# Kernel optimization log

Measured on AMD Instinct MI355X. Metric: run time of the kernel, lower is better.

## Reference

```python
import jax, jax.numpy as jnp
import numpy as np
from jax import lax

B, S, E = 1, 8192, 64
KSZ = 2
THRESHOLD = 0.0
GAMMA = 1.0
OUT_DIM = 4


def setup_inputs() -> dict:
    key = jax.random.key(0)
    ks = jax.random.split(key, 12)
    def lin(k, fan_in, fan_out):
        bound = 1.0 / np.sqrt(fan_in)
        kw, kb = jax.random.split(k)
        W = jax.random.uniform(kw, (fan_in, fan_out), jnp.float32, -bound, bound)
        b = jax.random.uniform(kb, (fan_out,), jnp.float32, -bound, bound)
        return W, b
    x = jax.random.normal(ks[0], (B, S, E), jnp.float32)
    cb = 1.0 / np.sqrt(KSZ * KSZ)
    conv_w = jax.random.uniform(ks[1], (1, 1, KSZ, KSZ), jnp.float32, -cb, cb)
    conv_b = jax.random.uniform(ks[2], (1,), jnp.float32, -cb, cb)
    Wq, bq = lin(ks[3], E, E)
    Wk, bk = lin(ks[4], E, E)
    Wv, bv = lin(ks[5], E, E)
    Wp, bp = lin(ks[6], E, OUT_DIM)
    return {"x": x, "conv_w": conv_w, "conv_b": conv_b, "Wq": Wq, "bq": bq,
            "Wk": Wk, "bk": bk, "Wv": Wv, "bv": bv, "Wp": Wp, "bp": bp}


def reference(x, conv_w, conv_b, Wq, bq, Wk, bk, Wv, bv, Wp, bp):
    # conv pre-filter: (B,S,E) -> (B,1,E,S) -> scalar per batch
    patched = jnp.transpose(x, (0, 2, 1))[:, None]  # (B,1,E,S)
    logits = lax.conv_general_dilated(
        patched, conv_w, (1, 1), "VALID",
        dimension_numbers=("NCHW", "OIHW", "NCHW")) + conv_b[None, :, None, None]
    conv_feat = jax.nn.sigmoid(logits - THRESHOLD).mean(axis=(2, 3))  # (B,1)
    conv_feat = conv_feat.reshape(B)[:, None]  # (B,1)

    # classical scaled dot-product attention (note: no output projection in source)
    scale = E ** (-0.5)
    q = x @ Wq + bq
    k = x @ Wk + bk
    v = x @ Wv + bv
    scores = jnp.einsum("bse,bte->bst", q, k) * scale  # (B,S,S)
    attn = jax.nn.softmax(scores, axis=-1)
    attn_out = jnp.einsum("bst,bte->bse", attn, v)  # (B,S,E)

    # RBF reweighting (identically 1 since x==y, computed faithfully)
    diff = attn_out - attn_out
    kernel_vals = jnp.exp(-GAMMA * jnp.sum(diff * diff, axis=-1, keepdims=True))  # (B,S,1)

    weighted = attn_out * conv_feat * kernel_vals  # broadcast valid since B==1
    pooled = weighted.mean(axis=1)  # (B,E)
    return pooled @ Wp + bp  # (B,4)
```

## Files before the change

kernel.cpp:

```cpp
#include <hip/hip_runtime.h>
#include <hip/hip_bf16.h>

#define S_LEN 8192
#define E_DIM 64
#define NCONV (63 * 8191)
#define KSPLIT 32
#define KRANGE (S_LEN / KSPLIT)
#define SVT (S_LEN + 32)
#define KTS 72

typedef short short8 __attribute__((ext_vector_type(8)));
typedef float f32x4 __attribute__((ext_vector_type(4)));

__device__ __forceinline__ float ldin(const void* __restrict__ p, int i, int f32flag) {
    return f32flag ? ((const float*)p)[i]
                   : __bfloat162float(((const __hip_bfloat16*)p)[i]);
}
__device__ __forceinline__ float bfbits2f(unsigned int u16bits) {
    union { unsigned int u; float f; } c; c.u = u16bits << 16; return c.f;
}
__device__ __forceinline__ unsigned short f2bfu(float f) {
    __hip_bfloat16 h = __float2bfloat16(f);
    union { __hip_bfloat16 h; unsigned short u; } c; c.h = h; return c.u;
}
__device__ __forceinline__ int hw_bad(unsigned short h) {
    const unsigned int e = (h >> 7) & 0xFF;
    return !(h == 0 || h == 0x8000 || (e >= 0x60 && e <= 0x86));
}

__global__ __launch_bounds__(256) void qkv_conv(
    const void* __restrict__ x,
    const void* __restrict__ conv_w, const void* __restrict__ conv_b,
    const void* __restrict__ Wq, const void* __restrict__ bq,
    const void* __restrict__ Wk, const void* __restrict__ bk,
    const void* __restrict__ Wv, const void* __restrict__ bv,
    unsigned short* __restrict__ q_bf, unsigned short* __restrict__ k_bf,
    unsigned short* __restrict__ vT_bf, float* __restrict__ conv_part,
    float* __restrict__ l_g, float* __restrict__ w_g,
    float* __restrict__ g_pooled, int* __restrict__ counter)
{
    __shared__ int s_fx, s_fw;
    const int tid = threadIdx.x;
    if (tid == 0) { s_fx = 0; s_fw = 0; }
    __syncthreads();
    if (tid < 64) { if (hw_bad(((const unsigned short*)x)[tid])) atomicOr(&s_fx, 1); }
    else if (tid < 128) { if (hw_bad(((const unsigned short*)Wq)[tid - 64])) atomicOr(&s_fw, 1); }
    __syncthreads();
    const int fx = s_fx, fw = s_fw;

    if (blockIdx.x >= 256) {
        const int bid = blockIdx.x - 256;
        const int gid = bid * 256 + tid;
        if (gid < 8192) { l_g[gid] = 0.f; w_g[gid] = 0.f; }
        if (gid < 64) g_pooled[gid] = 0.f;
        if (gid == 0) *counter = 0;
        const float c0 = ldin(conv_w, 0, fw), c1 = ldin(conv_w, 1, fw);
        const float c2 = ldin(conv_w, 2, fw), c3 = ldin(conv_w, 3, fw);
        const float cb = ldin(conv_b, 0, fw);
        float acc = 0.f;
        for (int idx = gid; idx < NCONV; idx += 64 * 256) {
            const int h = idx % 63;
            const int w = idx / 63;
            const float z = c0 * ldin(x, w * 64 + h, fx)     + c1 * ldin(x, (w + 1) * 64 + h, fx)
                          + c2 * ldin(x, w * 64 + h + 1, fx) + c3 * ldin(x, (w + 1) * 64 + h + 1, fx)
                          + cb;
            acc += 1.f / (1.f + __expf(-z));
        }
        for (int off = 32; off > 0; off >>= 1) acc += __shfl_down(acc, off);
        __shared__ float wsum[4];
        if ((tid & 63) == 0) wsum[tid >> 6] = acc;
        __syncthreads();
        if (tid == 0) conv_part[bid] = wsum[0] + wsum[1] + wsum[2] + wsum[3];
        return;
    }

    __shared__ float wsh[3][4096];
    __shared__ float xT[64 * 16];
    __shared__ float bsh[3][64];
    __shared__ float vs[64 * 17];
    const void* Ws[3] = { Wq, Wk, Wv };
    const void* Bs[3] = { bq, bk, bv };
#pragma unroll
    for (int w = 0; w < 3; ++w) {
        if (fw) {
            const float4* src = (const float4*)Ws[w];
            for (int i = tid; i < 1024; i += 256) {
                float4 v = src[i];
                float* d = &wsh[w][i * 4];
                d[0] = v.x; d[1] = v.y; d[2] = v.z; d[3] = v.w;
            }
            if (tid < 64) bsh[w][tid] = ((const float*)Bs[w])[tid];
        } else {
            const uint4* src = (const uint4*)Ws[w];
            for (int i = tid; i < 512; i += 256) {
                uint4 v = src[i];
                float* d = &wsh[w][i * 8];
                d[0] = bfbits2f(v.x & 0xffff); d[1] = bfbits2f(v.x >> 16);
                d[2] = bfbits2f(v.y & 0xffff); d[3] = bfbits2f(v.y >> 16);
                d[4] = bfbits2f(v.z & 0xffff); d[5] = bfbits2f(v.z >> 16);
                d[6] = bfbits2f(v.w & 0xffff); d[7] = bfbits2f(v.w >> 16);
            }
            if (tid < 64) bsh[w][tid] = bfbits2f(((const unsigned short*)Bs[w])[tid]);
        }
    }

#pragma unroll
    for (int ch = 0; ch < 2; ++ch) {
        const int row0 = blockIdx.x * 32 + ch * 16;
        __syncthreads();
        for (int idx = tid; idx < 1024; idx += 256) {
            const int r = idx >> 6, i = idx & 63;
            xT[i * 16 + r] = ldin(x, (row0 + r) * 64 + i, fx);
        }
        __syncthreads();

        const int e = tid & 63, rg = tid >> 6;
        float aq[4], ak[4], av[4];
#pragma unroll
        for (int r = 0; r < 4; ++r) { aq[r] = bsh[0][e]; ak[r] = bsh[1][e]; av[r] = bsh[2][e]; }
#pragma unroll 8
        for (int i = 0; i < 64; ++i) {
            const float4 xv = *(const float4*)&xT[i * 16 + rg * 4];
            const float wq = wsh[0][i * 64 + e], wk = wsh[1][i * 64 + e], wv = wsh[2][i * 64 + e];
            aq[0] += xv.x * wq; aq[1] += xv.y * wq; aq[2] += xv.z * wq; aq[3] += xv.w * wq;
            ak[0] += xv.x * wk; ak[1] += xv.y * wk; ak[2] += xv.z * wk; ak[3] += xv.w * wk;
            av[0] += xv.x * wv; av[1] += xv.y * wv; av[2] += xv.z * wv; av[3] += xv.w * wv;
        }
#pragma unroll
        for (int r = 0; r < 4; ++r) {
            const int row = row0 + rg * 4 + r;
            q_bf[row * 64 + e] = f2bfu(aq[r] * 0.125f);
            k_bf[row * 64 + e] = f2bfu(ak[r]);
            vs[e * 17 + rg * 4 + r] = av[r];
        }
        __syncthreads();
        {
            const int e2 = tid >> 2, rp = (tid & 3) * 4;
            const unsigned short h0 = f2bfu(vs[e2 * 17 + rp + 0]);
            const unsigned short h1 = f2bfu(vs[e2 * 17 + rp + 1]);
            const unsigned short h2 = f2bfu(vs[e2 * 17 + rp + 2]);
            const unsigned short h3 = f2bfu(vs[e2 * 17 + rp + 3]);
            uint2 pk;
            pk.x = (unsigned int)h0 | ((unsigned int)h1 << 16);
            pk.y = (unsigned int)h2 | ((unsigned int)h3 << 16);
            *(uint2*)(vT_bf + (size_t)e2 * SVT + row0 + rp) = pk;
        }
    }
}

__global__ __launch_bounds__(256) void attn_l(
    const unsigned short* __restrict__ q_bf, const unsigned short* __restrict__ k_bf,
    float* __restrict__ l_g)
{
    __shared__ unsigned short kt[2][32 * KTS];
    const int tid = threadIdx.x;
    const int wave = tid >> 6, lane = tid & 63;
    const int ln = lane & 15, quad = lane >> 4;
    const int qrow0 = blockIdx.x * 256 + wave * 64;
    const int kbase = blockIdx.y * KRANGE;

    short8 aQ[4][2];
#pragma unroll
    for (int T = 0; T < 4; ++T) {
        aQ[T][0] = *(const short8*)(q_bf + (qrow0 + 16 * T + ln) * 64 + quad * 8);
        aQ[T][1] = *(const short8*)(q_bf + (qrow0 + 16 * T + ln) * 64 + 32 + quad * 8);
    }
    const f32x4 zero = {0.f, 0.f, 0.f, 0.f};
    float l_acc[4][4];
#pragma unroll
    for (int T = 0; T < 4; ++T)
#pragma unroll
        for (int r = 0; r < 4; ++r) l_acc[T][r] = 0.f;

    const int krow = tid >> 3, kch = tid & 7;
    uint4 kreg;
    {
        const uint4 k0 = *(const uint4*)(k_bf + (size_t)(kbase + krow) * 64 + kch * 8);
        *(uint4*)(&kt[0][krow * KTS + kch * 8]) = k0;
        kreg = *(const uint4*)(k_bf + (size_t)(kbase + 32 + krow) * 64 + kch * 8);
    }
    __syncthreads();

    const int nIter = KRANGE >> 5;
#pragma unroll 2
    for (int kc = 0; kc < nIter; ++kc) {
        const int cur = kc & 1;
        if (kc + 1 < nIter) *(uint4*)(&kt[cur ^ 1][krow * KTS + kch * 8]) = kreg;
        if (kc + 2 < nIter)
            kreg = *(const uint4*)(k_bf + (size_t)(kbase + (kc + 2) * 32 + krow) * 64 + kch * 8);
        const unsigned short* ktc = &kt[cur][0];
        const short8 bE0 = *(const short8*)(ktc + (2 * ln) * KTS + quad * 8);
        const short8 bE1 = *(const short8*)(ktc + (2 * ln) * KTS + 32 + quad * 8);
        const short8 bO0 = *(const short8*)(ktc + (2 * ln + 1) * KTS + quad * 8);
        const short8 bO1 = *(const short8*)(ktc + (2 * ln + 1) * KTS + 32 + quad * 8);
        f32x4 scE[4], scO[4];
#pragma unroll
        for (int T = 0; T < 4; ++T) {
            scE[T] = __builtin_amdgcn_mfma_f32_16x16x32_bf16(aQ[T][0], bE0, zero, 0, 0, 0);
            scE[T] = __builtin_amdgcn_mfma_f32_16x16x32_bf16(aQ[T][1], bE1, scE[T], 0, 0, 0);
            scO[T] = __builtin_amdgcn_mfma_f32_16x16x32_bf16(aQ[T][0], bO0, zero, 0, 0, 0);
            scO[T] = __builtin_amdgcn_mfma_f32_16x16x32_bf16(aQ[T][1], bO1, scO[T], 0, 0, 0);
        }
#pragma unroll
        for (int T = 0; T < 4; ++T)
#pragma unroll
            for (int r = 0; r < 4; ++r)
                l_acc[T][r] += __expf(scE[T][r]) + __expf(scO[T][r]);
        __syncthreads();
    }

#pragma unroll
    for (int T = 0; T < 4; ++T)
#pragma unroll
        for (int r = 0; r < 4; ++r) {
            float v = l_acc[T][r];
            v += __shfl_xor(v, 1); v += __shfl_xor(v, 2);
            v += __shfl_xor(v, 4); v += __shfl_xor(v, 8);
            if (ln == 0) atomicAdd(&l_g[qrow0 + 16 * T + quad * 4 + r], v);
        }
}

__global__ __launch_bounds__(256) void attn_w(
    const unsigned short* __restrict__ q_bf, const unsigned short* __restrict__ k_bf,
    const float* __restrict__ l_g, float* __restrict__ w_g)
{
    __shared__ unsigned short kt[2][32 * KTS];
    __shared__ float w_sh[4][KRANGE];
    const int tid = threadIdx.x;
    const int wave = tid >> 6, lane = tid & 63;
    const int ln = lane & 15, quad = lane >> 4;
    const int qrow0 = blockIdx.x * 256 + wave * 64;
    const int kbase = blockIdx.y * KRANGE;

    short8 aQ[4][2];
    float lv[4][4];
#pragma unroll
    for (int T = 0; T < 4; ++T) {
        aQ[T][0] = *(const short8*)(q_bf + (qrow0 + 16 * T + ln) * 64 + quad * 8);
        aQ[T][1] = *(const short8*)(q_bf + (qrow0 + 16 * T + ln) * 64 + 32 + quad * 8);
#pragma unroll
        for (int r = 0; r < 4; ++r)
            lv[T][r] = 1.f / l_g[qrow0 + 16 * T + quad * 4 + r];
    }
    const f32x4 zero = {0.f, 0.f, 0.f, 0.f};

    const int krow = tid >> 3, kch = tid & 7;
    uint4 kreg;
    {
        const uint4 k0 = *(const uint4*)(k_bf + (size_t)(kbase + krow) * 64 + kch * 8);
        *(uint4*)(&kt[0][krow * KTS + kch * 8]) = k0;
        kreg = *(const uint4*)(k_bf + (size_t)(kbase + 32 + krow) * 64 + kch * 8);
    }
    __syncthreads();

    const int nIter = KRANGE >> 5;
#pragma unroll 2
    for (int kc = 0; kc < nIter; ++kc) {
        const int cur = kc & 1;
        if (kc + 1 < nIter) *(uint4*)(&kt[cur ^ 1][krow * KTS + kch * 8]) = kreg;
        if (kc + 2 < nIter)
            kreg = *(const uint4*)(k_bf + (size_t)(kbase + (kc + 2) * 32 + krow) * 64 + kch * 8);
        const unsigned short* ktc = &kt[cur][0];
        const short8 bE0 = *(const short8*)(ktc + (2 * ln) * KTS + quad * 8);
        const short8 bE1 = *(const short8*)(ktc + (2 * ln) * KTS + 32 + quad * 8);
        const short8 bO0 = *(const short8*)(ktc + (2 * ln + 1) * KTS + quad * 8);
        const short8 bO1 = *(const short8*)(ktc + (2 * ln + 1) * KTS + 32 + quad * 8);
        f32x4 scE[4], scO[4];
#pragma unroll
        for (int T = 0; T < 4; ++T) {
            scE[T] = __builtin_amdgcn_mfma_f32_16x16x32_bf16(aQ[T][0], bE0, zero, 0, 0, 0);
            scE[T] = __builtin_amdgcn_mfma_f32_16x16x32_bf16(aQ[T][1], bE1, scE[T], 0, 0, 0);
            scO[T] = __builtin_amdgcn_mfma_f32_16x16x32_bf16(aQ[T][0], bO0, zero, 0, 0, 0);
            scO[T] = __builtin_amdgcn_mfma_f32_16x16x32_bf16(aQ[T][1], bO1, scO[T], 0, 0, 0);
        }
        float wE = 0.f, wO = 0.f;
#pragma unroll
        for (int T = 0; T < 4; ++T)
#pragma unroll
            for (int r = 0; r < 4; ++r) {
                wE += __expf(scE[T][r]) * lv[T][r];
                wO += __expf(scO[T][r]) * lv[T][r];
            }
        wE += __shfl_xor(wE, 16); wE += __shfl_xor(wE, 32);
        wO += __shfl_xor(wO, 16); wO += __shfl_xor(wO, 32);
        if (lane < 16) {
            w_sh[wave][kc * 32 + 2 * ln]     = wE;
            w_sh[wave][kc * 32 + 2 * ln + 1] = wO;
        }
        __syncthreads();
    }

    for (int k = tid; k < KRANGE; k += 256)
        atomicAdd(&w_g[kbase + k], w_sh[0][k] + w_sh[1][k] + w_sh[2][k] + w_sh[3][k]);
}

__global__ __launch_bounds__(256) void gemv_final(
    const float* __restrict__ w_g, const unsigned short* __restrict__ vT_bf,
    float* __restrict__ g_pooled, int* __restrict__ counter,
    const float* __restrict__ conv_part,
    const void* __restrict__ Wp, const void* __restrict__ bp,
    const void* __restrict__ x, const void* __restrict__ Wq,
    void* __restrict__ out)
{
    __shared__ float psum[64][5];
    const int tid = threadIdx.x;
    const int e = tid >> 2, j = tid & 3;
    const int t0 = blockIdx.x * 256 + j * 64;
    float acc = 0.f;
#pragma unroll
    for (int i = 0; i < 8; ++i) {
        const uint4 v = *(const uint4*)(vT_bf + (size_t)e * SVT + t0 + i * 8);
        const float4 wa = *(const float4*)(w_g + t0 + i * 8);
        const float4 wb = *(const float4*)(w_g + t0 + i * 8 + 4);
        acc += wa.x * bfbits2f(v.x & 0xffff) + wa.y * bfbits2f(v.x >> 16)
             + wa.z * bfbits2f(v.y & 0xffff) + wa.w * bfbits2f(v.y >> 16)
             + wb.x * bfbits2f(v.z & 0xffff) + wb.y * bfbits2f(v.z >> 16)
             + wb.z * bfbits2f(v.w & 0xffff) + wb.w * bfbits2f(v.w >> 16);
    }
    psum[e][j] = acc;
    __syncthreads();
    if (j == 0) atomicAdd(&g_pooled[e], psum[e][0] + psum[e][1] + psum[e][2] + psum[e][3]);
    __threadfence();
    __shared__ int s_last;
    if (tid == 0) s_last = (atomicAdd(counter, 1) == 31) ? 1 : 0;
    __syncthreads();
    if (!s_last || tid >= 64) return;
    __threadfence();

    const int ee = tid;
    int badx = hw_bad(((const unsigned short*)x)[ee]);
    int badw = hw_bad(((const unsigned short*)Wq)[ee]);
    const int fx = (__ballot(badx) != 0ULL) ? 1 : 0;
    const int fw = (__ballot(badw) != 0ULL) ? 1 : 0;
    const int out_f32 = fx & fw;

    float cv = conv_part[ee];
    cv += __shfl_xor(cv, 1); cv += __shfl_xor(cv, 2); cv += __shfl_xor(cv, 4);
    cv += __shfl_xor(cv, 8); cv += __shfl_xor(cv, 16); cv += __shfl_xor(cv, 32);
    const float conv_feat = cv * (1.f / (float)NCONV);
    const float pe = atomicAdd(&g_pooled[ee], 0.f);
    const float pooled = pe * (1.f / (float)S_LEN) * conv_feat;
    float p0 = pooled * ldin(Wp, ee * 4 + 0, fw);
    float p1 = pooled * ldin(Wp, ee * 4 + 1, fw);
    float p2 = pooled * ldin(Wp, ee * 4 + 2, fw);
    float p3 = pooled * ldin(Wp, ee * 4 + 3, fw);
    for (int off = 32; off > 0; off >>= 1) {
        p0 += __shfl_down(p0, off);
        p1 += __shfl_down(p1, off);
        p2 += __shfl_down(p2, off);
        p3 += __shfl_down(p3, off);
    }
    if (ee == 0) {
        const float r0 = p0 + ldin(bp, 0, fw);
        const float r1 = p1 + ldin(bp, 1, fw);
        const float r2 = p2 + ldin(bp, 2, fw);
        const float r3 = p3 + ldin(bp, 3, fw);
        if (out_f32) {
            float* oo = (float*)out;
            oo[0] = r0; oo[1] = r1; oo[2] = r2; oo[3] = r3;
        } else {
            __hip_bfloat16* oo = (__hip_bfloat16*)out;
            oo[0] = __float2bfloat16(r0); oo[1] = __float2bfloat16(r1);
            oo[2] = __float2bfloat16(r2); oo[3] = __float2bfloat16(r3);
        }
    }
}

extern "C" void kernel_launch(void* const* d_in, const int* in_sizes, int n_in,
                              void* d_out, int out_size, void* d_ws, size_t ws_size,
                              hipStream_t stream)
{
    const void* x  = d_in[0];
    const void* cw = d_in[1];
    const void* cb = d_in[2];
    const void* Wq = d_in[3];
    const void* bq = d_in[4];
    const void* Wk = d_in[5];
    const void* bk = d_in[6];
    const void* Wv = d_in[7];
    const void* bv = d_in[8];
    const void* Wp = d_in[9];
    const void* bp = d_in[10];

    float* ws = (float*)d_ws;
    float* g_pooled  = ws;
    int*   counter   = (int*)(ws + 64);
    float* conv_part = ws + 128;
    float* l_g       = ws + 256;
    float* w_g       = ws + 256 + 8192;
    unsigned short* q_bf  = (unsigned short*)(ws + 256 + 2 * 8192);
    unsigned short* k_bf  = q_bf + (size_t)S_LEN * 64;
    unsigned short* vT_bf = k_bf + (size_t)S_LEN * 64;

    qkv_conv<<<320, 256, 0, stream>>>(x, cw, cb, Wq, bq, Wk, bk, Wv, bv,
                                      q_bf, k_bf, vT_bf, conv_part,
                                      l_g, w_g, g_pooled, counter);
    attn_l<<<dim3(32, KSPLIT), 256, 0, stream>>>(q_bf, k_bf, l_g);
    attn_w<<<dim3(32, KSPLIT), 256, 0, stream>>>(q_bf, k_bf, l_g, w_g);
    gemv_final<<<32, 256, 0, stream>>>(w_g, vT_bf, g_pooled, counter, conv_part,
                                       Wp, bp, x, Wq, d_out);
}
```

Measured before the change: 133.3 us.

## Fuse attention passes and final GEMV into one kernel with grid-wide spin barriers

Merges the row-sum pass, the weight pass and the final GEMV/projection into a single persistent kernel. Device-scope atomic counters with spin-waits replace the kernel boundaries between stages, which removes two launch gaps and tail drains. This relies on all 1024 blocks being co-resident (launch_bounds 256,4 on 256 CUs). If they are not, the kernel deadlocks, and spinning adds some overhead.

After: 414.9 us. +211.3%, slower.

```diff
diff --git a/kernel.cpp b/kernel.cpp
--- a/kernel.cpp
+++ b/kernel.cpp
@@ -26,6 +26,10 @@
 __device__ __forceinline__ int hw_bad(unsigned short h) {
     const unsigned int e = (h >> 7) & 0xFF;
     return !(h == 0 || h == 0x8000 || (e >= 0x60 && e <= 0x86));
+}
+__device__ __forceinline__ void spin_until(int* p, int target) {
+    while (__hip_atomic_load(p, __ATOMIC_RELAXED, __HIP_MEMORY_SCOPE_AGENT) < target)
+        __builtin_amdgcn_s_sleep(8);
 }
 
 __global__ __launch_bounds__(256) void qkv_conv(
@@ -37,7 +41,7 @@
     unsigned short* __restrict__ q_bf, unsigned short* __restrict__ k_bf,
     unsigned short* __restrict__ vT_bf, float* __restrict__ conv_part,
     float* __restrict__ l_g, float* __restrict__ w_g,
-    float* __restrict__ g_pooled, int* __restrict__ counter)
+    float* __restrict__ g_pooled, int* __restrict__ counters)
 {
     __shared__ int s_fx, s_fw;
     const int tid = threadIdx.x;
@@ -53,7 +57,7 @@
         const int gid = bid * 256 + tid;
         if (gid < 8192) { l_g[gid] = 0.f; w_g[gid] = 0.f; }
         if (gid < 64) g_pooled[gid] = 0.f;
-        if (gid == 0) *counter = 0;
+        if (gid < 4) counters[gid] = 0;
         const float c0 = ldin(conv_w, 0, fw), c1 = ldin(conv_w, 1, fw);
         const float c2 = ldin(conv_w, 2, fw), c3 = ldin(conv_w, 3, fw);
         const float cb = ldin(conv_b, 0, fw);
@@ -148,81 +152,15 @@
     }
 }
 
-__global__ __launch_bounds__(256) void attn_l(
+__global__ __launch_bounds__(256, 4) void attn_fused(
     const unsigned short* __restrict__ q_bf, const unsigned short* __restrict__ k_bf,
-    float* __restrict__ l_g)
-{
-    __shared__ unsigned short kt[2][32 * KTS];
-    const int tid = threadIdx.x;
-    const int wave = tid >> 6, lane = tid & 63;
-    const int ln = lane & 15, quad = lane >> 4;
-    const int qrow0 = blockIdx.x * 256 + wave * 64;
-    const int kbase = blockIdx.y * KRANGE;
-
-    short8 aQ[4][2];
-#pragma unroll
-    for (int T = 0; T < 4; ++T) {
-        aQ[T][0] = *(const short8*)(q_bf + (qrow0 + 16 * T + ln) * 64 + quad * 8);
-        aQ[T][1] = *(const short8*)(q_bf + (qrow0 + 16 * T + ln) * 64 + 32 + quad * 8);
-    }
-    const f32x4 zero = {0.f, 0.f, 0.f, 0.f};
-    float l_acc[4][4];
-#pragma unroll
-    for (int T = 0; T < 4; ++T)
-#pragma unroll
-        for (int r = 0; r < 4; ++r) l_acc[T][r] = 0.f;
-
-    const int krow = tid >> 3, kch = tid & 7;
-    uint4 kreg;
-    {
-        const uint4 k0 = *(const uint4*)(k_bf + (size_t)(kbase + krow) * 64 + kch * 8);
-        *(uint4*)(&kt[0][krow * KTS + kch * 8]) = k0;
-        kreg = *(const uint4*)(k_bf + (size_t)(kbase + 32 + krow) * 64 + kch * 8);
-    }
-    __syncthreads();
-
-    const int nIter = KRANGE >> 5;
-#pragma unroll 2
-    for (int kc = 0; kc < nIter; ++kc) {
-        const int cur = kc & 1;
-        if (kc + 1 < nIter) *(uint4*)(&kt[cur ^ 1][krow * KTS + kch * 8]) = kreg;
-        if (kc + 2 < nIter)
-            kreg = *(const uint4*)(k_bf + (size_t)(kbase + (kc + 2) * 32 + krow) * 64 + kch * 8);
-        const unsigned short* ktc = &kt[cur][0];
-        const short8 bE0 = *(const short8*)(ktc + (2 * ln) * KTS + quad * 8);
-        const short8 bE1 = *(const short8*)(ktc + (2 * ln) * KTS + 32 + quad * 8);
-        const short8 bO0 = *(const short8*)(ktc + (2 * ln + 1) * KTS + quad * 8);
-        const short8 bO1 = *(const short8*)(ktc + (2 * ln + 1) * KTS + 32 + quad * 8);
-        f32x4 scE[4], scO[4];
-#pragma unroll
-        for (int T = 0; T < 4; ++T) {
-            scE[T] = __builtin_amdgcn_mfma_f32_16x16x32_bf16(aQ[T][0], bE0, zero, 0, 0, 0);
-            scE[T] = __builtin_amdgcn_mfma_f32_16x16x32_bf16(aQ[T][1], bE1, scE[T], 0, 0, 0);
-            scO[T] = __builtin_amdgcn_mfma_f32_16x16x32_bf16(aQ[T][0], bO0, zero, 0, 0, 0);
-            scO[T] = __builtin_amdgcn_mfma_f32_16x16x32_bf16(aQ[T][1], bO1, scO[T], 0, 0, 0);
-        }
-#pragma unroll
-        for (int T = 0; T < 4; ++T)
-#pragma unroll
-            for (int r = 0; r < 4; ++r)
-                l_acc[T][r] += __expf(scE[T][r]) + __expf(scO[T][r]);
-        __syncthreads();
-    }
-
-#pragma unroll
-    for (int T = 0; T < 4; ++T)
-#pragma unroll
-        for (int r = 0; r < 4; ++r) {
-            float v = l_acc[T][r];
-            v += __shfl_xor(v, 1); v += __shfl_xor(v, 2);
-            v += __shfl_xor(v, 4); v += __shfl_xor(v, 8);
-            if (ln == 0) atomicAdd(&l_g[qrow0 + 16 * T + quad * 4 + r], v);
-        }
-}
-
-__global__ __launch_bounds__(256) void attn_w(
-    const unsigned short* __restrict__ q_bf, const unsigned short* __restrict__ k_bf,
-    const float* __restrict__ l_g, float* __restrict__ w_g)
+    const unsigned short* __restrict__ vT_bf,
+    float* __restrict__ l_g, float* __restrict__ w_g,
+    float* __restrict__ g_pooled, int* __restrict__ counters,
+    const float* __restrict__ conv_part,
+    const void* __restrict__ Wp, const void* __restrict__ bp,
+    const void* __restrict__ x, const void* __restrict__ Wq,
+    void* __restrict__ out)
 {
     __shared__ unsigned short kt[2][32 * KTS];
     __shared__ float w_sh[4][KRANGE];
@@ -231,103 +169,162 @@
     const int ln = lane & 15, quad = lane >> 4;
     const int qrow0 = blockIdx.x * 256 + wave * 64;
     const int kbase = blockIdx.y * KRANGE;
+    const f32x4 zero = {0.f, 0.f, 0.f, 0.f};
+    const int krow = tid >> 3, kch = tid & 7;
 
     short8 aQ[4][2];
-    float lv[4][4];
 #pragma unroll
     for (int T = 0; T < 4; ++T) {
         aQ[T][0] = *(const short8*)(q_bf + (qrow0 + 16 * T + ln) * 64 + quad * 8);
         aQ[T][1] = *(const short8*)(q_bf + (qrow0 + 16 * T + ln) * 64 + 32 + quad * 8);
-#pragma unroll
-        for (int r = 0; r < 4; ++r)
-            lv[T][r] = 1.f / l_g[qrow0 + 16 * T + quad * 4 + r];
-    }
-    const f32x4 zero = {0.f, 0.f, 0.f, 0.f};
-
-    const int krow = tid >> 3, kch = tid & 7;
-    uint4 kreg;
+    }
+
     {
-        const uint4 k0 = *(const uint4*)(k_bf + (size_t)(kbase + krow) * 64 + kch * 8);
-        *(uint4*)(&kt[0][krow * KTS + kch * 8]) = k0;
-        kreg = *(const uint4*)(k_bf + (size_t)(kbase + 32 + krow) * 64 + kch * 8);
-    }
-    __syncthreads();
-
-    const int nIter = KRANGE >> 5;
+        float l_acc[4][4];
+#pragma unroll
+        for (int T = 0; T < 4; ++T)
+#pragma unroll
+            for (int r = 0; r < 4; ++r) l_acc[T][r] = 0.f;
+        uint4 kreg;
+        {
+            const uint4 k0 = *(const uint4*)(k_bf + (size_t)(kbase + krow) * 64 + kch * 8);
+            *(uint4*)(&kt[0][krow * KTS + kch * 8]) = k0;
+            kreg = *(const uint4*)(k_bf + (size_t)(kbase + 32 + krow) * 64 + kch * 8);
+        }
+        __syncthreads();
+        const int nIter = KRANGE >> 5;
 #pragma unroll 2
-    for (int kc = 0; kc < nIter; ++kc) {
-        const int cur = kc & 1;
-        if (kc + 1 < nIter) *(uint4*)(&kt[cur ^ 1][krow * KTS + kch * 8]) = kreg;
-        if (kc + 2 < nIter)
-            kreg = *(const uint4*)(k_bf + (size_t)(kbase + (kc + 2) * 32 + krow) * 64 + kch * 8);
-        const unsigned short* ktc = &kt[cur][0];
-        const short8 bE0 = *(const short8*)(ktc + (2 * ln) * KTS + quad * 8);
-        const short8 bE1 = *(const short8*)(ktc + (2 * ln) * KTS + 32 + quad * 8);
-        const short8 bO0 = *(const short8*)(ktc + (2 * ln + 1) * KTS + quad * 8);
-        const short8 bO1 = *(const short8*)(ktc + (2 * ln + 1) * KTS + 32 + quad * 8);
-        f32x4 scE[4], scO[4];
-#pragma unroll
-        for (int T = 0; T < 4; ++T) {
-            scE[T] = __builtin_amdgcn_mfma_f32_16x16x32_bf16(aQ[T][0], bE0, zero, 0, 0, 0);
-            scE[T] = __builtin_amdgcn_mfma_f32_16x16x32_bf16(aQ[T][1], bE1, scE[T], 0, 0, 0);
-            scO[T] = __builtin_amdgcn_mfma_f32_16x16x32_bf16(aQ[T][0], bO0, zero, 0, 0, 0);
-            scO[T] = __builtin_amdgcn_mfma_f32_16x16x32_bf16(aQ[T][1], bO1, scO[T], 0, 0, 0);
-        }
-        float wE = 0.f, wO = 0.f;
+        for (int kc = 0; kc < nIter; ++kc) {
+            const int cur = kc & 1;
+            if (kc + 1 < nIter) *(uint4*)(&kt[cur ^ 1][krow * KTS + kch * 8]) = kreg;
+            if (kc + 2 < nIter)
+                kreg = *(const uint4*)(k_bf + (size_t)(kbase + (kc + 2) * 32 + krow) * 64 + kch * 8);
+            const unsigned short* ktc = &kt[cur][0];
+            const short8 bE0 = *(const short8*)(ktc + (2 * ln) * KTS + quad * 8);
+            const short8 bE1 = *(const short8*)(ktc + (2 * ln) * KTS + 32 + quad * 8);
+            const short8 bO0 = *(const short8*)(ktc + (2 * ln + 1) * KTS + quad * 8);
+            const short8 bO1 = *(const short8*)(ktc + (2 * ln + 1) * KTS + 32 + quad * 8);
+            f32x4 scE[4], scO[4];
+#pragma unroll
+            for (int T = 0; T < 4; ++T) {
+                scE[T] = __builtin_amdgcn_mfma_f32_16x16x32_bf16(aQ[T][0], bE0, zero, 0, 0, 0);
+                scE[T] = __builtin_amdgcn_mfma_f32_16x16x32_bf16(aQ[T][1], bE1, scE[T], 0, 0, 0);
+                scO[T] = __builtin_amdgcn_mfma_f32_16x16x32_bf16(aQ[T][0], bO0, zero, 0, 0, 0);
+                scO[T] = __builtin_amdgcn_mfma_f32_16x16x32_bf16(aQ[T][1], bO1, scO[T], 0, 0, 0);
+            }
+#pragma unroll
+            for (int T = 0; T < 4; ++T)
+#pragma unroll
+                for (int r = 0; r < 4; ++r)
+                    l_acc[T][r] += __expf(scE[T][r]) + __expf(scO[T][r]);
+            __syncthreads();
+        }
 #pragma unroll
         for (int T = 0; T < 4; ++T)
 #pragma unroll
             for (int r = 0; r < 4; ++r) {
-                wE += __expf(scE[T][r]) * lv[T][r];
-                wO += __expf(scO[T][r]) * lv[T][r];
-            }
-        wE += __shfl_xor(wE, 16); wE += __shfl_xor(wE, 32);
-        wO += __shfl_xor(wO, 16); wO += __shfl_xor(wO, 32);
-        if (lane < 16) {
-            w_sh[wave][kc * 32 + 2 * ln]     = wE;
-            w_sh[wave][kc * 32 + 2 * ln + 1] = wO;
-        }
-        __syncthreads();
-    }
-
-    for (int k = tid; k < KRANGE; k += 256)
-        atomicAdd(&w_g[kbase + k], w_sh[0][k] + w_sh[1][k] + w_sh[2][k] + w_sh[3][k]);
-}
-
-__global__ __launch_bounds__(256) void gemv_final(
-    const float* __restrict__ w_g, const unsigned short* __restrict__ vT_bf,
-    float* __restrict__ g_pooled, int* __restrict__ counter,
-    const float* __restrict__ conv_part,
-    const void* __restrict__ Wp, const void* __restrict__ bp,
-    const void* __restrict__ x, const void* __restrict__ Wq,
-    void* __restrict__ out)
-{
+                float v = l_acc[T][r];
+                v += __shfl_xor(v, 1); v += __shfl_xor(v, 2);
+                v += __shfl_xor(v, 4); v += __shfl_xor(v, 8);
+                if (ln == 0) atomicAdd(&l_g[qrow0 + 16 * T + quad * 4 + r], v);
+            }
+    }
+
+    __threadfence();
+    if (tid == 0) { atomicAdd(&counters[0], 1); spin_until(&counters[0], 1024); }
+    __syncthreads();
+    __threadfence();
+
+    {
+        float lv[4][4];
+#pragma unroll
+        for (int T = 0; T < 4; ++T)
+#pragma unroll
+            for (int r = 0; r < 4; ++r)
+                lv[T][r] = 1.f / l_g[qrow0 + 16 * T + quad * 4 + r];
+        uint4 kreg;
+        {
+            const uint4 k0 = *(const uint4*)(k_bf + (size_t)(kbase + krow) * 64 + kch * 8);
+            *(uint4*)(&kt[0][krow * KTS + kch * 8]) = k0;
+            kreg = *(const uint4*)(k_bf + (size_t)(kbase + 32 + krow) * 64 + kch * 8);
+        }
+        __syncthreads();
+        const int nIter = KRANGE >> 5;
+#pragma unroll 2
+        for (int kc = 0; kc < nIter; ++kc) {
+            const int cur = kc & 1;
+            if (kc + 1 < nIter) *(uint4*)(&kt[cur ^ 1][krow * KTS + kch * 8]) = kreg;
+            if (kc + 2 < nIter)
+                kreg = *(const uint4*)(k_bf + (size_t)(kbase + (kc + 2) * 32 + krow) * 64 + kch * 8);
+            const unsigned short* ktc = &kt[cur][0];
+            const short8 bE0 = *(const short8*)(ktc + (2 * ln) * KTS + quad * 8);
+            const short8 bE1 = *(const short8*)(ktc + (2 * ln) * KTS + 32 + quad * 8);
+            const short8 bO0 = *(const short8*)(ktc + (2 * ln + 1) * KTS + quad * 8);
+            const short8 bO1 = *(const short8*)(ktc + (2 * ln + 1) * KTS + 32 + quad * 8);
+            f32x4 scE[4], scO[4];
+#pragma unroll
+            for (int T = 0; T < 4; ++T) {
+                scE[T] = __builtin_amdgcn_mfma_f32_16x16x32_bf16(aQ[T][0], bE0, zero, 0, 0, 0);
+                scE[T] = __builtin_amdgcn_mfma_f32_16x16x32_bf16(aQ[T][1], bE1, scE[T], 0, 0, 0);
+                scO[T] = __builtin_amdgcn_mfma_f32_16x16x32_bf16(aQ[T][0], bO0, zero, 0, 0, 0);
+                scO[T] = __builtin_amdgcn_mfma_f32_16x16x32_bf16(aQ[T][1], bO1, scO[T], 0, 0, 0);
+            }
+            float wE = 0.f, wO = 0.f;
+#pragma unroll
+            for (int T = 0; T < 4; ++T)
+#pragma unroll
+                for (int r = 0; r < 4; ++r) {
+                    wE += __expf(scE[T][r]) * lv[T][r];
+                    wO += __expf(scO[T][r]) * lv[T][r];
+                }
+            wE += __shfl_xor(wE, 16); wE += __shfl_xor(wE, 32);
+            wO += __shfl_xor(wO, 16); wO += __shfl_xor(wO, 32);
+            if (lane < 16) {
+                w_sh[wave][kc * 32 + 2 * ln]     = wE;
+                w_sh[wave][kc * 32 + 2 * ln + 1] = wO;
+            }
+            __syncthreads();
+        }
+        for (int k = tid; k < KRANGE; k += 256)
+            atomicAdd(&w_g[kbase + k], w_sh[0][k] + w_sh[1][k] + w_sh[2][k] + w_sh[3][k]);
+    }
+
+    __threadfence();
+    if (tid == 0) atomicAdd(&counters[1], 1);
+    if (blockIdx.x != 0) return;
+    if (tid == 0) spin_until(&counters[1], 1024);
+    __syncthreads();
+    __threadfence();
+
     __shared__ float psum[64][5];
-    const int tid = threadIdx.x;
-    const int e = tid >> 2, j = tid & 3;
-    const int t0 = blockIdx.x * 256 + j * 64;
-    float acc = 0.f;
-#pragma unroll
-    for (int i = 0; i < 8; ++i) {
-        const uint4 v = *(const uint4*)(vT_bf + (size_t)e * SVT + t0 + i * 8);
-        const float4 wa = *(const float4*)(w_g + t0 + i * 8);
-        const float4 wb = *(const float4*)(w_g + t0 + i * 8 + 4);
-        acc += wa.x * bfbits2f(v.x & 0xffff) + wa.y * bfbits2f(v.x >> 16)
-             + wa.z * bfbits2f(v.y & 0xffff) + wa.w * bfbits2f(v.y >> 16)
-             + wb.x * bfbits2f(v.z & 0xffff) + wb.y * bfbits2f(v.z >> 16)
-             + wb.z * bfbits2f(v.w & 0xffff) + wb.w * bfbits2f(v.w >> 16);
-    }
-    psum[e][j] = acc;
-    __syncthreads();
-    if (j == 0) atomicAdd(&g_pooled[e], psum[e][0] + psum[e][1] + psum[e][2] + psum[e][3]);
-    __threadfence();
-    __shared__ int s_last;
-    if (tid == 0) s_last = (atomicAdd(counter, 1) == 31) ? 1 : 0;
-    __syncthreads();
-    if (!s_last || tid >= 64) return;
-    __threadfence();
+    {
+        const int e = tid >> 2, j = tid & 3;
+        const int t0 = kbase + j * 64;
+        float acc = 0.f;
+#pragma unroll
+        for (int i = 0; i < 8; ++i) {
+            const uint4 v = *(const uint4*)(vT_bf + (size_t)e * SVT + t0 + i * 8);
+            const float4 wa = *(const float4*)(w_g + t0 + i * 8);
+            const float4 wb = *(const float4*)(w_g + t0 + i * 8 + 4);
+            acc += wa.x * bfbits2f(v.x & 0xffff) + wa.y * bfbits2f(v.x >> 16)
+                 + wa.z * bfbits2f(v.y & 0xffff) + wa.w * bfbits2f(v.y >> 16)
+                 + wb.x * bfbits2f(v.z & 0xffff) + wb.y * bfbits2f(v.z >> 16)
+                 + wb.z * bfbits2f(v.w & 0xffff) + wb.w * bfbits2f(v.w >> 16);
+        }
+        psum[e][j] = acc;
+    }
+    __syncthreads();
+    if (tid < 64) atomicAdd(&g_pooled[tid], psum[tid][0] + psum[tid][1] + psum[tid][2] + psum[tid][3]);
+    __threadfence();
+    if (tid == 0) atomicAdd(&counters[2], 1);
+    if (blockIdx.y != 0) return;
+    if (tid == 0) spin_until(&counters[2], 32);
+    __syncthreads();
+    __threadfence();
+    if (tid >= 64) return;
 
     const int ee = tid;
+    const float pe = atomicAdd(&g_pooled[ee], 0.f);
     int badx = hw_bad(((const unsigned short*)x)[ee]);
     int badw = hw_bad(((const unsigned short*)Wq)[ee]);
     const int fx = (__ballot(badx) != 0ULL) ? 1 : 0;
@@ -338,7 +335,6 @@
     cv += __shfl_xor(cv, 1); cv += __shfl_xor(cv, 2); cv += __shfl_xor(cv, 4);
     cv += __shfl_xor(cv, 8); cv += __shfl_xor(cv, 16); cv += __shfl_xor(cv, 32);
     const float conv_feat = cv * (1.f / (float)NCONV);
-    const float pe = atomicAdd(&g_pooled[ee], 0.f);
     const float pooled = pe * (1.f / (float)S_LEN) * conv_feat;
     float p0 = pooled * ldin(Wp, ee * 4 + 0, fw);
     float p1 = pooled * ldin(Wp, ee * 4 + 1, fw);
@@ -384,7 +380,7 @@
 
     float* ws = (float*)d_ws;
     float* g_pooled  = ws;
-    int*   counter   = (int*)(ws + 64);
+    int*   counters  = (int*)(ws + 64);
     float* conv_part = ws + 128;
     float* l_g       = ws + 256;
     float* w_g       = ws + 256 + 8192;
@@ -394,9 +390,8 @@
 
     qkv_conv<<<320, 256, 0, stream>>>(x, cw, cb, Wq, bq, Wk, bk, Wv, bv,
                                       q_bf, k_bf, vT_bf, conv_part,
-                                      l_g, w_g, g_pooled, counter);
-    attn_l<<<dim3(32, KSPLIT), 256, 0, stream>>>(q_bf, k_bf, l_g);
-    attn_w<<<dim3(32, KSPLIT), 256, 0, stream>>>(q_bf, k_bf, l_g, w_g);
-    gemv_final<<<32, 256, 0, stream>>>(w_g, vT_bf, g_pooled, counter, conv_part,
-                                       Wp, bp, x, Wq, d_out);
-}
+                                      l_g, w_g, g_pooled, counters);
+    attn_fused<<<dim3(32, KSPLIT), 256, 0, stream>>>(
+        q_bf, k_bf, vT_bf, l_g, w_g, g_pooled, counters, conv_part,
+        Wp, bp, x, Wq, d_out);
+}
```
